# Optimization experiments

Hardware: AMD Instinct MI355X
Metric: run time of the kernel (lower is better)

## Reference

```python
import jax, jax.numpy as jnp
import numpy as np

KERNEL_MUL = 2.0
KERNEL_NUM = 5
SIZE = 128  # hardcoded slice size in the original forward


def setup_inputs() -> dict:
    key = jax.random.key(0)
    k1, k2 = jax.random.split(key)
    B, D, S = 64, 4096, 128
    source = jax.random.normal(k1, (B, D, S), dtype=jnp.float32)
    target = jax.random.normal(k2, (B, D, S), dtype=jnp.float32)
    return {"source": source, "target": target}


def _mmd_rbf(source, target):
    # source/target: [B, D, S] with S == SIZE
    B, D, S = source.shape
    # per-sample: permute to [S, D] and concat -> total: [B, 2S, D]
    x = jnp.concatenate(
        [jnp.transpose(source, (0, 2, 1)), jnp.transpose(target, (0, 2, 1))], axis=1
    )
    n = 2 * S
    sq = jnp.sum(x * x, axis=-1)  # [B, 2S]
    # pairwise squared L2 via Gram matrix (avoids [2S,2S,D] expansion)
    gram = jnp.einsum("bnd,bmd->bnm", x, x)  # [B, 2S, 2S]
    L2 = sq[:, :, None] + sq[:, None, :] - 2.0 * gram  # [B, 2S, 2S]
    # bandwidth from detached distances (torch uses L2_distance.data)
    bw = jax.lax.stop_gradient(jnp.sum(L2, axis=(1, 2))) / (n * n - n)  # [B]
    bw = bw / (KERNEL_MUL ** (KERNEL_NUM // 2))
    scales = KERNEL_MUL ** jnp.arange(KERNEL_NUM, dtype=jnp.float32)  # [K]
    bws = bw[:, None, None, None] * scales[None, :, None, None]  # [B, K, 1, 1]
    kernels = jnp.sum(jnp.exp(-L2[:, None, :, :] / bws), axis=1)  # [B, 2S, 2S]
    K = jnp.mean(kernels, axis=0)  # sum over batch / B -> [2S, 2S]
    loss = (
        jnp.mean(K[:SIZE, :SIZE])
        + jnp.mean(K[SIZE:, SIZE:])
        - jnp.mean(K[:SIZE, SIZE:])
        - jnp.mean(K[SIZE:, :SIZE])
    )
    return loss


def reference(source, target):
    return _mmd_rbf(source, target)
```

## Files before the change

kernel.cpp:

```cpp
#include <hip/hip_runtime.h>

#define B_  64
#define D_  4096
#define S_  128
#define N_  256
#define KC_ 4
#define KPB (D_ / KC_)
#define BK  64
#define NCH (KPB / BK)
#define RS  72
#define LDSBUF (N_ * RS)
#define TILE_ (N_ * N_)

using short8   = __attribute__((ext_vector_type(8)))  short;
using floatx16 = __attribute__((ext_vector_type(16))) float;

__device__ __forceinline__ unsigned int pk2(float lo, float hi) {
  unsigned int r;
  asm("v_cvt_pk_bf16_f32 %0, %1, %2" : "=v"(r) : "v"(lo), "v"(hi));
  return r;
}

__device__ __forceinline__ int swz(int n, int g) {
  return n * RS + ((g ^ ((n >> 3) & 3)) << 3);
}

__global__ __launch_bounds__(1024, 4) void k_gram(
    const float* __restrict__ src, const float* __restrict__ tgt,
    float* __restrict__ partial, float* __restrict__ tot,
    float* __restrict__ sq) {
  __shared__ unsigned short lds[2 * LDSBUF];
  __shared__ float red[16];
  const int kc  = blockIdx.x;
  const int b   = blockIdx.y;
  const int tid = threadIdx.x;
  const int l   = tid & 63;
  const int w   = tid >> 6;
  const int wr  = w >> 2;
  const int wc  = w & 3;

  const int n_s = tid & 255;
  const int g   = tid >> 8;
  const float* colbase = (n_s < S_)
      ? (src + (size_t)b * D_ * S_ + n_s)
      : (tgt + (size_t)b * D_ * S_ + (n_s - S_));
  const float* pA = colbase + (size_t)kc * KPB * S_;

  float ld[16];
  floatx16 acc[2][2];
  #pragma unroll
  for (int i = 0; i < 2; i++)
    #pragma unroll
    for (int j = 0; j < 2; j++)
      #pragma unroll
      for (int r = 0; r < 16; r++) acc[i][j][r] = 0.f;

  const int lm   = l & 31;
  const int lk   = l >> 5;
  const int ar   = wr * 64 + lm;
  const int bcol = wc * 64 + lm;

  #define LOADH(ch)                                                    \
    do {                                                               \
      const float* q = pA + (size_t)(ch) * BK * S_;                    \
      _Pragma("unroll")                                                \
      for (int j = 0; j < 8; j++) {                                    \
        ld[j]     = q[(size_t)(g * 8 + j) * S_];                       \
        ld[8 + j] = q[(size_t)((g + 4) * 8 + j) * S_];                 \
      }                                                                \
    } while (0)

  #define WRITEH(buf)                                                  \
    do {                                                               \
      uint4 wa, wb;                                                    \
      wa.x = pk2(ld[0],  ld[1]);                                       \
      wa.y = pk2(ld[2],  ld[3]);                                       \
      wa.z = pk2(ld[4],  ld[5]);                                       \
      wa.w = pk2(ld[6],  ld[7]);                                       \
      wb.x = pk2(ld[8],  ld[9]);                                       \
      wb.y = pk2(ld[10], ld[11]);                                      \
      wb.z = pk2(ld[12], ld[13]);                                      \
      wb.w = pk2(ld[14], ld[15]);                                      \
      const int base_ = (buf) * LDSBUF;                                \
      *(uint4*)&lds[base_ + swz(n_s, g)]     = wa;                     \
      *(uint4*)&lds[base_ + swz(n_s, g + 4)] = wb;                     \
    } while (0)

  #define MFMAH(buf, k0)                                               \
    do {                                                               \
      const unsigned short* L = &lds[(buf) * LDSBUF];                  \
      _Pragma("unroll")                                                \
      for (int ks = (k0); ks < (k0) + 2; ks++) {                       \
        const int gg = ks * 2 + lk;                                    \
        short8 a0 = *(const short8*)&L[swz(ar,        gg)];            \
        short8 a1 = *(const short8*)&L[swz(ar + 32,   gg)];            \
        short8 b0 = *(const short8*)&L[swz(bcol,      gg)];            \
        short8 b1 = *(const short8*)&L[swz(bcol + 32, gg)];            \
        acc[0][0] = __builtin_amdgcn_mfma_f32_32x32x16_bf16(a0, b0, acc[0][0], 0, 0, 0); \
        acc[0][1] = __builtin_amdgcn_mfma_f32_32x32x16_bf16(a0, b1, acc[0][1], 0, 0, 0); \
        acc[1][0] = __builtin_amdgcn_mfma_f32_32x32x16_bf16(a1, b0, acc[1][0], 0, 0, 0); \
        acc[1][1] = __builtin_amdgcn_mfma_f32_32x32x16_bf16(a1, b1, acc[1][1], 0, 0, 0); \
      }                                                                \
    } while (0)

  LOADH(0);
  WRITEH(0);
  LOADH(1);
  __syncthreads();
  for (int ch = 0; ch < NCH - 1; ch++) {
    MFMAH(ch & 1, 0);
    WRITEH((ch + 1) & 1);
    if (ch + 2 < NCH) LOADH(ch + 2);
    MFMAH(ch & 1, 2);
    __syncthreads();
  }
  MFMAH((NCH - 1) & 1, 0);
  MFMAH((NCH - 1) & 1, 2);

  float* gb = partial + ((size_t)kc * B_ + b) * TILE_;
  #pragma unroll
  for (int i = 0; i < 2; i++)
    #pragma unroll
    for (int j = 0; j < 2; j++)
      #pragma unroll
      for (int r = 0; r < 16; r++) {
        const int row = (r & 3) + 8 * (r >> 2) + 4 * lk;
        const int nr  = wr * 64 + i * 32 + row;
        const int nc  = wc * 64 + j * 32 + (l & 31);
        gb[nr * N_ + nc] = acc[i][j][r];
      }

  float s = 0.f;
  #pragma unroll
  for (int i = 0; i < 2; i++)
    #pragma unroll
    for (int j = 0; j < 2; j++)
      #pragma unroll
      for (int r = 0; r < 16; r++) s += acc[i][j][r];
  for (int off = 32; off; off >>= 1) s += __shfl_down(s, off);
  if (l == 0) red[w] = s;
  __syncthreads();
  if (tid == 0) {
    float T = 0.f;
    #pragma unroll
    for (int i = 0; i < 16; i++) T += red[i];
    atomicAdd(&tot[b], T);
  }

  if (wr == wc && lk == ((l >> 2) & 1)) {
    const int c = l & 31;
    const int r = (c >> 3) * 4 + (c & 3);
    #pragma unroll
    for (int i = 0; i < 2; i++)
      atomicAdd(&sq[b * N_ + wr * 64 + i * 32 + c], acc[i][i][r]);
  }
  #undef LOADH
  #undef WRITEH
  #undef MFMAH
}

__global__ __launch_bounds__(512, 4) void k_exp(
    const float* __restrict__ partial, const float* __restrict__ tot,
    const float* __restrict__ sq, float* __restrict__ out) {
  __shared__ float sqs[N_];
  __shared__ float red[8];
  __shared__ float bws;
  const int rc = blockIdx.x;
  const int b  = blockIdx.y;
  const int t  = threadIdx.x;
  const int cg = t & 63;
  const int rg = t >> 6;

  if (t < N_) sqs[t] = sq[b * N_ + t];
  __syncthreads();
  if (t < N_) {
    float v = sqs[t];
    for (int off = 32; off; off >>= 1) v += __shfl_down(v, off);
    if ((t & 63) == 0) red[t >> 6] = v;
  }
  __syncthreads();
  if (t == 0) {
    float ssq = red[0] + red[1] + red[2] + red[3];
    float SL2 = 2.f * (float)N_ * ssq - 2.f * tot[b];
    bws = SL2 / (float)(N_ * N_ - N_) * 0.25f;
  }
  __syncthreads();

  const float bwv = bws;
  float nb[5];
  #pragma unroll
  for (int k = 0; k < 5; k++)
    nb[k] = -1.4426950408889634f / (bwv * (float)(1 << k));

  const int c4 = cg * 4;
  const float4 sqc = *(const float4*)&sqs[c4];
  const float sgn = ((rc < 4) == (cg < 32)) ? 1.f : -1.f;
  const float* p0 = partial + (size_t)b * TILE_;

  float accv = 0.f;
  #pragma unroll
  for (int r = 0; r < 4; r++) {
    const int row = rc * 32 + rg * 4 + r;
    const float4 g0 = *(const float4*)&p0[row * N_ + c4];
    const float4 g1 = *(const float4*)&p0[(size_t)1 * B_ * TILE_ + row * N_ + c4];
    const float4 g2 = *(const float4*)&p0[(size_t)2 * B_ * TILE_ + row * N_ + c4];
    const float4 g3 = *(const float4*)&p0[(size_t)3 * B_ * TILE_ + row * N_ + c4];
    const float sr = sqs[row];
    float4 L2;
    L2.x = sr + sqc.x - 2.f * (g0.x + g1.x + g2.x + g3.x);
    L2.y = sr + sqc.y - 2.f * (g0.y + g1.y + g2.y + g3.y);
    L2.z = sr + sqc.z - 2.f * (g0.z + g1.z + g2.z + g3.z);
    L2.w = sr + sqc.w - 2.f * (g0.w + g1.w + g2.w + g3.w);
    #pragma unroll
    for (int k = 0; k < 5; k++) {
      accv += exp2f(L2.x * nb[k]) + exp2f(L2.y * nb[k])
            + exp2f(L2.z * nb[k]) + exp2f(L2.w * nb[k]);
    }
  }
  accv *= sgn;
  for (int off = 32; off; off >>= 1) accv += __shfl_down(accv, off);
  __syncthreads();
  if ((t & 63) == 0) red[t >> 6] = accv;
  __syncthreads();
  if (t == 0) {
    float s2 = red[0] + red[1] + red[2] + red[3]
             + red[4] + red[5] + red[6] + red[7];
    atomicAdd(out, s2 * (1.0f / (64.f * 16384.f)));
  }
}

extern "C" void kernel_launch(void* const* d_in, const int* in_sizes, int n_in,
                              void* d_out, int out_size, void* d_ws, size_t ws_size,
                              hipStream_t stream) {
  const float* src = (const float*)d_in[0];
  const float* tgt = (const float*)d_in[1];
  const size_t partial_bytes = (size_t)KC_ * B_ * TILE_ * sizeof(float);
  float* partial = (float*)d_ws;
  float* tot     = (float*)((char*)d_ws + partial_bytes);
  float* sq      = tot + B_;
  hipMemsetAsync(tot, 0, (B_ + B_ * N_) * sizeof(float), stream);
  hipMemsetAsync(d_out, 0, sizeof(float), stream);
  k_gram<<<dim3(KC_, B_), 1024, 0, stream>>>(src, tgt, partial, tot, sq);
  k_exp<<<dim3(8, B_), 512, 0, stream>>>(partial, tot, sq, (float*)d_out);
}
```

Baseline: 309.9 us.

## Split bandwidth reduction into its own kernel and double exp-kernel grid

```diff
diff --git a/kernel.cpp b/kernel.cpp
--- a/kernel.cpp
+++ b/kernel.cpp
@@ -24,6 +24,14 @@
 __device__ __forceinline__ int swz(int n, int g) {
   return n * RS + ((g ^ ((n >> 3) & 3)) << 3);
 }
+
+#define SYNC_LDS()                                                     \
+  do {                                                                 \
+    __builtin_amdgcn_sched_barrier(0);                                 \
+    asm volatile("s_waitcnt lgkmcnt(0)" ::: "memory");                 \
+    __builtin_amdgcn_s_barrier();                                      \
+    __builtin_amdgcn_sched_barrier(0);                                 \
+  } while (0)
 
 __global__ __launch_bounds__(1024, 4) void k_gram(
     const float* __restrict__ src, const float* __restrict__ tgt,
@@ -112,7 +120,7 @@
     WRITEH((ch + 1) & 1);
     if (ch + 2 < NCH) LOADH(ch + 2);
     MFMAH(ch & 1, 2);
-    __syncthreads();
+    SYNC_LDS();
   }
   MFMAH((NCH - 1) & 1, 0);
   MFMAH((NCH - 1) & 1, 2);
@@ -159,12 +167,28 @@
   #undef MFMAH
 }
 
+__global__ __launch_bounds__(256, 8) void k_bw(
+    const float* __restrict__ tot, const float* __restrict__ sq,
+    float* __restrict__ bws) {
+  __shared__ float red[4];
+  const int b = blockIdx.x;
+  const int t = threadIdx.x;
+  float v = sq[b * N_ + t];
+  for (int off = 32; off; off >>= 1) v += __shfl_down(v, off);
+  if ((t & 63) == 0) red[t >> 6] = v;
+  __syncthreads();
+  if (t == 0) {
+    float ssq = red[0] + red[1] + red[2] + red[3];
+    float SL2 = 2.f * (float)N_ * ssq - 2.f * tot[b];
+    bws[b] = SL2 / (float)(N_ * N_ - N_) * 0.25f;
+  }
+}
+
 __global__ __launch_bounds__(512, 4) void k_exp(
-    const float* __restrict__ partial, const float* __restrict__ tot,
+    const float* __restrict__ partial, const float* __restrict__ bws,
     const float* __restrict__ sq, float* __restrict__ out) {
   __shared__ float sqs[N_];
   __shared__ float red[8];
-  __shared__ float bws;
   const int rc = blockIdx.x;
   const int b  = blockIdx.y;
   const int t  = threadIdx.x;
@@ -173,20 +197,8 @@
 
   if (t < N_) sqs[t] = sq[b * N_ + t];
   __syncthreads();
-  if (t < N_) {
-    float v = sqs[t];
-    for (int off = 32; off; off >>= 1) v += __shfl_down(v, off);
-    if ((t & 63) == 0) red[t >> 6] = v;
-  }
-  __syncthreads();
-  if (t == 0) {
-    float ssq = red[0] + red[1] + red[2] + red[3];
-    float SL2 = 2.f * (float)N_ * ssq - 2.f * tot[b];
-    bws = SL2 / (float)(N_ * N_ - N_) * 0.25f;
-  }
-  __syncthreads();
-
-  const float bwv = bws;
+
+  const float bwv = bws[b];
   float nb[5];
   #pragma unroll
   for (int k = 0; k < 5; k++)
@@ -194,13 +206,13 @@
 
   const int c4 = cg * 4;
   const float4 sqc = *(const float4*)&sqs[c4];
-  const float sgn = ((rc < 4) == (cg < 32)) ? 1.f : -1.f;
+  const float sgn = ((rc < 8) == (cg < 32)) ? 1.f : -1.f;
   const float* p0 = partial + (size_t)b * TILE_;
 
   float accv = 0.f;
   #pragma unroll
-  for (int r = 0; r < 4; r++) {
-    const int row = rc * 32 + rg * 4 + r;
+  for (int r = 0; r < 2; r++) {
+    const int row = rc * 16 + rg * 2 + r;
     const float4 g0 = *(const float4*)&p0[row * N_ + c4];
     const float4 g1 = *(const float4*)&p0[(size_t)1 * B_ * TILE_ + row * N_ + c4];
     const float4 g2 = *(const float4*)&p0[(size_t)2 * B_ * TILE_ + row * N_ + c4];
@@ -219,7 +231,6 @@
   }
   accv *= sgn;
   for (int off = 32; off; off >>= 1) accv += __shfl_down(accv, off);
-  __syncthreads();
   if ((t & 63) == 0) red[t >> 6] = accv;
   __syncthreads();
   if (t == 0) {
@@ -238,8 +249,10 @@
   float* partial = (float*)d_ws;
   float* tot     = (float*)((char*)d_ws + partial_bytes);
   float* sq      = tot + B_;
+  float* bws     = sq + B_ * N_;
   hipMemsetAsync(tot, 0, (B_ + B_ * N_) * sizeof(float), stream);
   hipMemsetAsync(d_out, 0, sizeof(float), stream);
   k_gram<<<dim3(KC_, B_), 1024, 0, stream>>>(src, tgt, partial, tot, sq);
-  k_exp<<<dim3(8, B_), 512, 0, stream>>>(partial, tot, sq, (float*)d_out);
-}
+  k_bw<<<B_, 256, 0, stream>>>(tot, sq, bws);
+  k_exp<<<dim3(16, B_), 512, 0, stream>>>(partial, bws, sq, (float*)d_out);
+}
```

After: 315.1 us. No clear change (+1.7%).
